# Kernel optimization log

Hardware: AMD Instinct MI355X
Metric: run time of the kernel (lower is better)

Reference implementation:

```python
import jax, jax.numpy as jnp
import numpy as np

BN_EPS = 1e-5

def _bn_train(h, gamma, beta):
    # BatchNorm1d in training mode: biased batch stats over the edge (batch) dim
    mean = jnp.mean(h, axis=0)
    var = jnp.var(h, axis=0)
    return (h - mean) * jax.lax.rsqrt(var + BN_EPS) * gamma + beta

def setup_inputs() -> dict:
    key = jax.random.key(0)
    ks = jax.random.split(key, 8)
    N, C, E = 50000, 128, 600000
    x = jax.random.normal(ks[0], (N, C), dtype=jnp.float32)
    edge_index = jax.random.randint(ks[1], (2, E), 0, N, dtype=jnp.int64)
    # Linear params, Kaiming-uniform-ish scale (values don't matter for correctness)
    def lin(k, fan_in, fan_out):
        k1, k2 = jax.random.split(k)
        bound = 1.0 / np.sqrt(fan_in)
        W = jax.random.uniform(k1, (fan_out, fan_in), jnp.float32, -bound, bound)
        b = jax.random.uniform(k2, (fan_out,), jnp.float32, -bound, bound)
        return W, b
    W1, b1 = lin(ks[2], 2 * C, C)
    W2, b2 = lin(ks[3], C, C)
    W3, b3 = lin(ks[4], C, 1)
    g1 = jnp.ones((C,), jnp.float32); be1 = jnp.zeros((C,), jnp.float32)
    g2 = jnp.ones((C,), jnp.float32); be2 = jnp.zeros((C,), jnp.float32)
    return {"x": x, "edge_index": edge_index,
            "W1": W1, "b1": b1, "g1": g1, "be1": be1,
            "W2": W2, "b2": b2, "g2": g2, "be2": be2,
            "W3": W3, "b3": b3}

def reference(x, edge_index, W1, b1, g1, be1, W2, b2, g2, be2, W3, b3):
    # gather endpoint features and concat: [E, 2C]
    ef = jnp.concatenate([x[edge_index[0]], x[edge_index[1]]], axis=1)
    h = jnp.einsum('ec,oc->eo', ef, W1) + b1          # [E, C]
    h = jax.nn.relu(_bn_train(h, g1, be1))
    h = jnp.einsum('ec,oc->eo', h, W2) + b2           # [E, C]
    h = jax.nn.relu(_bn_train(h, g2, be2))
    h = jnp.einsum('ec,oc->eo', h, W3) + b3           # [E, 1]
    return jnp.squeeze(h)                             # [E]
```

## Files before the change

kernel.cpp:

```cpp
#include <hip/hip_runtime.h>
#include <hip/hip_bf16.h>

#define CH 128

constexpr float BN_EPS = 1e-5f;

typedef short bf16x8 __attribute__((ext_vector_type(8)));
typedef float f32x4  __attribute__((ext_vector_type(4)));

__device__ __forceinline__ unsigned cvtpk_bf16(float lo, float hi) {
    unsigned r;
    asm("v_cvt_pk_bf16_f32 %0, %1, %2" : "=v"(r) : "v"(lo), "v"(hi));
    return r;
}
__device__ __forceinline__ float bf2f_lo(unsigned u) { return __uint_as_float(u << 16); }
__device__ __forceinline__ float bf2f_hi(unsigned u) { return __uint_as_float(u & 0xffff0000u); }

union BF8 { bf16x8 v; unsigned u[4]; };

__device__ __forceinline__ bf16x8 pack8(float f0, float f1, float f2, float f3,
                                        float f4, float f5, float f6, float f7) {
    BF8 r;
    r.u[0] = cvtpk_bf16(f0, f1);
    r.u[1] = cvtpk_bf16(f2, f3);
    r.u[2] = cvtpk_bf16(f4, f5);
    r.u[3] = cvtpk_bf16(f6, f7);
    return r.v;
}

__global__ __launch_bounds__(512, 4) void node_linear_kernel(
    const float* __restrict__ x, const float* __restrict__ W1,
    unsigned short* __restrict__ u_bf, unsigned short* __restrict__ v_bf, int N)
{
    __shared__ short xs[64 * 128];

    const int t = threadIdx.x;
    const int lane = t & 63;
    const int wv = t >> 6;
    const int l15 = lane & 15;
    const int l4 = lane >> 4;
    const int n0 = blockIdx.x * 64;

    bf16x8 wfrag[2][4];
    #pragma unroll
    for (int ot = 0; ot < 2; ++ot) {
        const int o_ = wv * 32 + ot * 16 + l15;
        const float* wrow = (o_ < 128) ? (W1 + (size_t)o_ * 256)
                                       : (W1 + (size_t)(o_ - 128) * 256 + 128);
        #pragma unroll
        for (int kk = 0; kk < 4; ++kk) {
            float4 a = *(const float4*)(wrow + kk * 32 + l4 * 8);
            float4 b = *(const float4*)(wrow + kk * 32 + l4 * 8 + 4);
            wfrag[ot][kk] = pack8(a.x, a.y, a.z, a.w, b.x, b.y, b.z, b.w);
        }
    }

    const int c16 = t & 15;
    const int cb = c16 * 8;
    const int nsl = t >> 4;
    #pragma unroll
    for (int nn = 0; nn < 2; ++nn) {
        const int n_loc = nsl + nn * 32;
        const int n = n0 + n_loc;
        bf16x8 xv = {0, 0, 0, 0, 0, 0, 0, 0};
        if (n < N) {
            float4 a = *(const float4*)(x + (size_t)n * CH + cb);
            float4 b = *(const float4*)(x + (size_t)n * CH + cb + 4);
            xv = pack8(a.x, a.y, a.z, a.w, b.x, b.y, b.z, b.w);
        }
        *(bf16x8*)(xs + n_loc * 128 + (c16 ^ (n_loc & 7)) * 8) = xv;
    }
    __syncthreads();

    unsigned short* ob = (wv < 4) ? u_bf : v_bf;
    const int chb = (wv & 3) * 32;

    #pragma unroll
    for (int g = 0; g < 4; ++g) {
        const int nrow = g * 16 + l15;
        f32x4 D0 = {0.f, 0.f, 0.f, 0.f};
        f32x4 D1 = {0.f, 0.f, 0.f, 0.f};
        #pragma unroll
        for (int kk = 0; kk < 4; ++kk) {
            bf16x8 a = *(const bf16x8*)(xs + nrow * 128 + ((kk * 4 + l4) ^ (l15 & 7)) * 8);
            D0 = __builtin_amdgcn_mfma_f32_16x16x32_bf16(a, wfrag[0][kk], D0, 0, 0, 0);
            D1 = __builtin_amdgcn_mfma_f32_16x16x32_bf16(a, wfrag[1][kk], D1, 0, 0, 0);
        }
        #pragma unroll
        for (int r = 0; r < 4; ++r) {
            const int n = n0 + g * 16 + l4 * 4 + r;
            if (n < N) {
                unsigned pk = cvtpk_bf16(D0[r], D1[r]);
                ob[(size_t)n * CH + chb + l15]      = (unsigned short)pk;
                ob[(size_t)n * CH + chb + 16 + l15] = (unsigned short)(pk >> 16);
            }
        }
    }
}

__global__ __launch_bounds__(256) void stats1_kernel(
    const unsigned short* __restrict__ u_bf, const unsigned short* __restrict__ v_bf,
    const int* __restrict__ src, const int* __restrict__ dst,
    float* __restrict__ partials, int E)
{
    const int t = threadIdx.x;
    const int c8 = t & 31;
    const int eslot = t >> 5;
    const uint2* u2 = (const uint2*)u_bf;
    const uint2* v2 = (const uint2*)v_bf;

    float rs0=0.f, rs1=0.f, rs2=0.f, rs3=0.f;
    float rq0=0.f, rq1=0.f, rq2=0.f, rq3=0.f;

    const int iters = (E + 7) >> 3;
    for (int it = blockIdx.x; it < iters; it += gridDim.x) {
        int e = it * 8 + eslot;
        if (e < E) {
            int s = src[e], d = dst[e];
            uint2 a = u2[(size_t)s * 32 + c8];
            uint2 b = v2[(size_t)d * 32 + c8];
            float h0 = bf2f_lo(a.x) + bf2f_lo(b.x);
            float h1 = bf2f_hi(a.x) + bf2f_hi(b.x);
            float h2 = bf2f_lo(a.y) + bf2f_lo(b.y);
            float h3 = bf2f_hi(a.y) + bf2f_hi(b.y);
            rs0 += h0; rq0 += h0 * h0;
            rs1 += h1; rq1 += h1 * h1;
            rs2 += h2; rq2 += h2 * h2;
            rs3 += h3; rq3 += h3 * h3;
        }
    }
    __shared__ float red[256];
    red[t] = 0.f;
    __syncthreads();
    int c = c8 * 4;
    atomicAdd(&red[c + 0], rs0); atomicAdd(&red[c + 1], rs1);
    atomicAdd(&red[c + 2], rs2); atomicAdd(&red[c + 3], rs3);
    atomicAdd(&red[128 + c + 0], rq0); atomicAdd(&red[128 + c + 1], rq1);
    atomicAdd(&red[128 + c + 2], rq2); atomicAdd(&red[128 + c + 3], rq3);
    __syncthreads();
    partials[(size_t)blockIdx.x * 256 + t] = red[t];
}

__global__ __launch_bounds__(1024) void finalize_kernel(
    const float* __restrict__ partials, int nblocks,
    const float* __restrict__ gamma, const float* __restrict__ beta,
    const float* __restrict__ bias,
    float* __restrict__ scale, float* __restrict__ shift, float invE)
{
    __shared__ float accs[1024], accq[1024];
    const int t = threadIdx.x;
    const int ch = t & 127;
    const int sl = t >> 7;
    float s = 0.f, q = 0.f;
    for (int b = sl; b < nblocks; b += 8) {
        s += partials[(size_t)b * 256 + ch];
        q += partials[(size_t)b * 256 + 128 + ch];
    }
    accs[t] = s; accq[t] = q;
    __syncthreads();
    if (t < 128) {
        float st = 0.f, qt = 0.f;
        #pragma unroll
        for (int k = 0; k < 8; ++k) { st += accs[k * 128 + t]; qt += accq[k * 128 + t]; }
        const float m0 = st * invE;
        const float var = fmaxf(qt * invE - m0 * m0, 0.f);
        const float mean = m0 + (bias ? bias[t] : 0.f);
        const float sc = gamma[t] * rsqrtf(var + BN_EPS);
        scale[t] = sc;
        shift[t] = beta[t] - mean * sc;
    }
}

__global__ __launch_bounds__(512, 4) void layer2_kernel(
    const unsigned short* __restrict__ u_bf, const unsigned short* __restrict__ v_bf,
    const int* __restrict__ src, const int* __restrict__ dst,
    const float* __restrict__ b1,
    const float* __restrict__ scale1, const float* __restrict__ shift1,
    const float* __restrict__ W2, const float* __restrict__ b2,
    uint2* __restrict__ h2raw, float* __restrict__ partials, int E)
{
    __shared__ short ybuf[64 * 128];
    __shared__ float red[256];

    const int t = threadIdx.x;
    const int lane = t & 63;
    const int wv = t >> 6;
    const int p = wv & 3;
    const int h = wv >> 2;
    const int l15 = lane & 15;
    const int l4  = lane >> 4;

    bf16x8 wfrag[2][4];
    #pragma unroll
    for (int ot = 0; ot < 2; ++ot) {
        const int o = p * 32 + ot * 16 + l15;
        #pragma unroll
        for (int kk = 0; kk < 4; ++kk) {
            const float* wp = W2 + (size_t)o * CH + kk * 32 + l4 * 8;
            float4 a = *(const float4*)wp;
            float4 bq = *(const float4*)(wp + 4);
            wfrag[ot][kk] = pack8(a.x, a.y, a.z, a.w, bq.x, bq.y, bq.z, bq.w);
        }
    }
    float b2r[2][4];
    #pragma unroll
    for (int ot = 0; ot < 2; ++ot)
        #pragma unroll
        for (int r = 0; r < 4; ++r)
            b2r[ot][r] = b2[p * 32 + ot * 16 + l4 * 4 + r];

    const int c16 = t & 15;
    const int cb = c16 * 8;
    const int ebase = t >> 4;
    const float4 sca = *(const float4*)(scale1 + cb);
    const float4 scb = *(const float4*)(scale1 + cb + 4);
    const float4 sha = *(const float4*)(shift1 + cb);
    const float4 shb = *(const float4*)(shift1 + cb + 4);
    const float4 b1a = *(const float4*)(b1 + cb);
    const float4 b1b = *(const float4*)(b1 + cb + 4);
    float4 bsa, bsb;
    bsa.x = b1a.x*sca.x + sha.x; bsa.y = b1a.y*sca.y + sha.y;
    bsa.z = b1a.z*sca.z + sha.z; bsa.w = b1a.w*sca.w + sha.w;
    bsb.x = b1b.x*scb.x + shb.x; bsb.y = b1b.y*scb.y + shb.y;
    bsb.z = b1b.z*scb.z + shb.z; bsb.w = b1b.w*scb.w + shb.w;

    float rs[2][4] = {{0.f,0.f,0.f,0.f},{0.f,0.f,0.f,0.f}};
    float rq[2][4] = {{0.f,0.f,0.f,0.f},{0.f,0.f,0.f,0.f}};

    const int ntiles = (E + 63) >> 6;
    for (int tile = blockIdx.x; tile < ntiles; tile += gridDim.x) {
        __syncthreads();
        #pragma unroll
        for (int ee = 0; ee < 2; ++ee) {
            const int e_loc = ebase + ee * 32;
            const int e = tile * 64 + e_loc;
            bf16x8 y8 = {0, 0, 0, 0, 0, 0, 0, 0};
            if (e < E) {
                const int s = src[e], d = dst[e];
                const uint4 ua = *(const uint4*)(u_bf + (size_t)s * CH + cb);
                const uint4 va = *(const uint4*)(v_bf + (size_t)d * CH + cb);
                const float f0 = bf2f_lo(ua.x) + bf2f_lo(va.x);
                const float f1 = bf2f_hi(ua.x) + bf2f_hi(va.x);
                const float f2 = bf2f_lo(ua.y) + bf2f_lo(va.y);
                const float f3 = bf2f_hi(ua.y) + bf2f_hi(va.y);
                const float f4 = bf2f_lo(ua.z) + bf2f_lo(va.z);
                const float f5 = bf2f_hi(ua.z) + bf2f_hi(va.z);
                const float f6 = bf2f_lo(ua.w) + bf2f_lo(va.w);
                const float f7 = bf2f_hi(ua.w) + bf2f_hi(va.w);
                y8 = pack8(fmaxf(f0 * sca.x + bsa.x, 0.f),
                           fmaxf(f1 * sca.y + bsa.y, 0.f),
                           fmaxf(f2 * sca.z + bsa.z, 0.f),
                           fmaxf(f3 * sca.w + bsa.w, 0.f),
                           fmaxf(f4 * scb.x + bsb.x, 0.f),
                           fmaxf(f5 * scb.y + bsb.y, 0.f),
                           fmaxf(f6 * scb.z + bsb.z, 0.f),
                           fmaxf(f7 * scb.w + bsb.w, 0.f));
            }
            *(bf16x8*)(ybuf + e_loc * 128 + (c16 ^ (e_loc & 7)) * 8) = y8;
        }
        __syncthreads();

        #pragma unroll
        for (int g2 = 0; g2 < 2; ++g2) {
            const int g = h * 2 + g2;
            const int erow = g * 16 + l15;
            f32x4 D0 = {0.f, 0.f, 0.f, 0.f};
            f32x4 D1 = {0.f, 0.f, 0.f, 0.f};
            #pragma unroll
            for (int kk = 0; kk < 4; ++kk) {
                bf16x8 yf = *(const bf16x8*)(ybuf + erow * 128 + ((kk * 4 + l4) ^ (l15 & 7)) * 8);
                D0 = __builtin_amdgcn_mfma_f32_16x16x32_bf16(wfrag[0][kk], yf, D0, 0, 0, 0);
                D1 = __builtin_amdgcn_mfma_f32_16x16x32_bf16(wfrag[1][kk], yf, D1, 0, 0, 0);
            }
            const int gblk = tile * 4 + g;
            const bool ev = ((size_t)gblk * 16 + l15) < (size_t)E;
            {
                const float a0 = D0[0] + b2r[0][0], a1 = D0[1] + b2r[0][1];
                const float a2 = D0[2] + b2r[0][2], a3 = D0[3] + b2r[0][3];
                rs[0][0] += ev ? a0 : 0.f; rq[0][0] += ev ? a0 * a0 : 0.f;
                rs[0][1] += ev ? a1 : 0.f; rq[0][1] += ev ? a1 * a1 : 0.f;
                rs[0][2] += ev ? a2 : 0.f; rq[0][2] += ev ? a2 * a2 : 0.f;
                rs[0][3] += ev ? a3 : 0.f; rq[0][3] += ev ? a3 * a3 : 0.f;
                h2raw[((size_t)gblk * 8 + p * 2 + 0) * 64 + lane] =
                    make_uint2(cvtpk_bf16(a0, a1), cvtpk_bf16(a2, a3));
            }
            {
                const float c0 = D1[0] + b2r[1][0], c1 = D1[1] + b2r[1][1];
                const float c2 = D1[2] + b2r[1][2], c3 = D1[3] + b2r[1][3];
                rs[1][0] += ev ? c0 : 0.f; rq[1][0] += ev ? c0 * c0 : 0.f;
                rs[1][1] += ev ? c1 : 0.f; rq[1][1] += ev ? c1 * c1 : 0.f;
                rs[1][2] += ev ? c2 : 0.f; rq[1][2] += ev ? c2 * c2 : 0.f;
                rs[1][3] += ev ? c3 : 0.f; rq[1][3] += ev ? c3 * c3 : 0.f;
                h2raw[((size_t)gblk * 8 + p * 2 + 1) * 64 + lane] =
                    make_uint2(cvtpk_bf16(c0, c1), cvtpk_bf16(c2, c3));
            }
        }
    }

    __syncthreads();
    if (t < 256) red[t] = 0.f;
    __syncthreads();
    #pragma unroll
    for (int ot = 0; ot < 2; ++ot) {
        #pragma unroll
        for (int r = 0; r < 4; ++r) {
            float a = rs[ot][r], b = rq[ot][r];
            #pragma unroll
            for (int m = 1; m <= 8; m <<= 1) {
                a += __shfl_xor(a, m, 64);
                b += __shfl_xor(b, m, 64);
            }
            if (l15 == 0) {
                const int ch = p * 32 + ot * 16 + l4 * 4 + r;
                atomicAdd(&red[ch], a);
                atomicAdd(&red[128 + ch], b);
            }
        }
    }
    __syncthreads();
    if (t < 256) partials[(size_t)blockIdx.x * 256 + t] = red[t];
}

__global__ __launch_bounds__(256) void output_kernel(
    const uint2* __restrict__ h2raw,
    const float* __restrict__ scale2, const float* __restrict__ shift2,
    const float* __restrict__ W3, const float* __restrict__ b3,
    float* __restrict__ out, int E)
{
    __shared__ float sc_s[128], sh_s[128], w3_s[128];
    const int t = threadIdx.x;
    if (t < 128) { sc_s[t] = scale2[t]; sh_s[t] = shift2[t]; w3_s[t] = W3[t]; }
    __syncthreads();
    const int wv = t >> 6;
    const int lane = t & 63;
    const int l15 = lane & 15;
    const int l4 = lane >> 4;
    const float bias = b3[0];
    const int ngrp = (E + 15) >> 4;
    for (int g = blockIdx.x * 4 + wv; g < ngrp; g += gridDim.x * 4) {
        float acc = 0.f;
        #pragma unroll
        for (int w = 0; w < 8; ++w) {
            uint2 raw = h2raw[((size_t)g * 8 + w) * 64 + lane];
            const int o = w * 16 + l4 * 4;
            float4 sc = *(const float4*)(sc_s + o);
            float4 sh = *(const float4*)(sh_s + o);
            float4 w3 = *(const float4*)(w3_s + o);
            float h0 = bf2f_lo(raw.x), h1 = bf2f_hi(raw.x);
            float h2 = bf2f_lo(raw.y), h3 = bf2f_hi(raw.y);
            acc += fmaxf(h0 * sc.x + sh.x, 0.f) * w3.x;
            acc += fmaxf(h1 * sc.y + sh.y, 0.f) * w3.y;
            acc += fmaxf(h2 * sc.z + sh.z, 0.f) * w3.z;
            acc += fmaxf(h3 * sc.w + sh.w, 0.f) * w3.w;
        }
        acc += __shfl_xor(acc, 16, 64);
        acc += __shfl_xor(acc, 32, 64);
        const int e = g * 16 + l15;
        if (l4 == 0 && e < E) out[e] = acc + bias;
    }
}

extern "C" void kernel_launch(void* const* d_in, const int* in_sizes, int n_in,
                              void* d_out, int out_size, void* d_ws, size_t ws_size,
                              hipStream_t stream)
{
    const float* x   = (const float*)d_in[0];
    const int*   ei  = (const int*)d_in[1];
    const float* W1  = (const float*)d_in[2];
    const float* b1  = (const float*)d_in[3];
    const float* g1  = (const float*)d_in[4];
    const float* be1 = (const float*)d_in[5];
    const float* W2  = (const float*)d_in[6];
    const float* b2  = (const float*)d_in[7];
    const float* g2  = (const float*)d_in[8];
    const float* be2 = (const float*)d_in[9];
    const float* W3  = (const float*)d_in[10];
    const float* b3  = (const float*)d_in[11];

    const int N = in_sizes[0] / CH;
    const int E = out_size;
    const int* src = ei;
    const int* dst = ei + E;

    const int S1_BLOCKS = 2048;
    const int S2_BLOCKS = 1024;
    const size_t ngblk = (size_t)((E + 63) >> 6) * 4;

    unsigned short* u_bf = (unsigned short*)d_ws;
    unsigned short* v_bf = u_bf + (size_t)N * CH;
    uint2* h2raw = (uint2*)(v_bf + (size_t)N * CH);
    float* part1 = (float*)(h2raw + ngblk * 8 * 64);
    float* part2 = part1 + (size_t)S1_BLOCKS * 256;
    float* scale1 = part2 + (size_t)S2_BLOCKS * 256;
    float* shift1 = scale1 + CH;
    float* scale2 = shift1 + CH;
    float* shift2 = scale2 + CH;
    float* out = (float*)d_out;

    node_linear_kernel<<<(N + 63) / 64, 512, 0, stream>>>(x, W1, u_bf, v_bf, N);
    stats1_kernel<<<S1_BLOCKS, 256, 0, stream>>>(u_bf, v_bf, src, dst, part1, E);
    finalize_kernel<<<1, 1024, 0, stream>>>(part1, S1_BLOCKS, g1, be1, b1,
                                            scale1, shift1, 1.0f / (float)E);
    layer2_kernel<<<S2_BLOCKS, 512, 0, stream>>>(u_bf, v_bf, src, dst, b1, scale1, shift1,
                                                 W2, b2, h2raw, part2, E);
    finalize_kernel<<<1, 1024, 0, stream>>>(part2, S2_BLOCKS, g2, be2, nullptr,
                                            scale2, shift2, 1.0f / (float)E);
    output_kernel<<<2048, 256, 0, stream>>>(h2raw, scale2, shift2, W3, b3, out, E);
}
```

Measured before the change: 314.1 us.

## Prefetch next-tile gathers with double-buffered LDS in layer2; unroll stats and output loops

```diff
diff --git a/kernel.cpp b/kernel.cpp
--- a/kernel.cpp
+++ b/kernel.cpp
@@ -15,6 +15,10 @@
 }
 __device__ __forceinline__ float bf2f_lo(unsigned u) { return __uint_as_float(u << 16); }
 __device__ __forceinline__ float bf2f_hi(unsigned u) { return __uint_as_float(u & 0xffff0000u); }
+
+__device__ __forceinline__ void lds_barrier() {
+    asm volatile("s_waitcnt lgkmcnt(0)\n\ts_barrier" ::: "memory");
+}
 
 union BF8 { bf16x8 v; unsigned u[4]; };
 
@@ -112,27 +116,35 @@
     float rs0=0.f, rs1=0.f, rs2=0.f, rs3=0.f;
     float rq0=0.f, rq1=0.f, rq2=0.f, rq3=0.f;
 
-    const int iters = (E + 7) >> 3;
+    const int iters = (E + 15) >> 4;
     for (int it = blockIdx.x; it < iters; it += gridDim.x) {
-        int e = it * 8 + eslot;
-        if (e < E) {
-            int s = src[e], d = dst[e];
-            uint2 a = u2[(size_t)s * 32 + c8];
-            uint2 b = v2[(size_t)d * 32 + c8];
-            float h0 = bf2f_lo(a.x) + bf2f_lo(b.x);
-            float h1 = bf2f_hi(a.x) + bf2f_hi(b.x);
-            float h2 = bf2f_lo(a.y) + bf2f_lo(b.y);
-            float h3 = bf2f_hi(a.y) + bf2f_hi(b.y);
-            rs0 += h0; rq0 += h0 * h0;
-            rs1 += h1; rq1 += h1 * h1;
-            rs2 += h2; rq2 += h2 * h2;
-            rs3 += h3; rq3 += h3 * h3;
+        const int e0 = it * 16 + eslot;
+        const int e1 = e0 + 8;
+        if (e0 < E) {
+            const int s = src[e0], d = dst[e0];
+            const uint2 a = u2[(size_t)s * 32 + c8];
+            const uint2 b = v2[(size_t)d * 32 + c8];
+            float h;
+            h = bf2f_lo(a.x) + bf2f_lo(b.x); rs0 += h; rq0 += h * h;
+            h = bf2f_hi(a.x) + bf2f_hi(b.x); rs1 += h; rq1 += h * h;
+            h = bf2f_lo(a.y) + bf2f_lo(b.y); rs2 += h; rq2 += h * h;
+            h = bf2f_hi(a.y) + bf2f_hi(b.y); rs3 += h; rq3 += h * h;
+        }
+        if (e1 < E) {
+            const int s = src[e1], d = dst[e1];
+            const uint2 a = u2[(size_t)s * 32 + c8];
+            const uint2 b = v2[(size_t)d * 32 + c8];
+            float h;
+            h = bf2f_lo(a.x) + bf2f_lo(b.x); rs0 += h; rq0 += h * h;
+            h = bf2f_hi(a.x) + bf2f_hi(b.x); rs1 += h; rq1 += h * h;
+            h = bf2f_lo(a.y) + bf2f_lo(b.y); rs2 += h; rq2 += h * h;
+            h = bf2f_hi(a.y) + bf2f_hi(b.y); rs3 += h; rq3 += h * h;
         }
     }
     __shared__ float red[256];
     red[t] = 0.f;
     __syncthreads();
-    int c = c8 * 4;
+    const int c = c8 * 4;
     atomicAdd(&red[c + 0], rs0); atomicAdd(&red[c + 1], rs1);
     atomicAdd(&red[c + 2], rs2); atomicAdd(&red[c + 3], rs3);
     atomicAdd(&red[128 + c + 0], rq0); atomicAdd(&red[128 + c + 1], rq1);
@@ -179,7 +191,7 @@
     const float* __restrict__ W2, const float* __restrict__ b2,
     uint2* __restrict__ h2raw, float* __restrict__ partials, int E)
 {
-    __shared__ short ybuf[64 * 128];
+    __shared__ short ybuf[2][64 * 128];
     __shared__ float red[256];
 
     const int t = threadIdx.x;
@@ -228,25 +240,37 @@
     float rq[2][4] = {{0.f,0.f,0.f,0.f},{0.f,0.f,0.f,0.f}};
 
     const int ntiles = (E + 63) >> 6;
-    for (int tile = blockIdx.x; tile < ntiles; tile += gridDim.x) {
-        __syncthreads();
-        #pragma unroll
-        for (int ee = 0; ee < 2; ++ee) {
-            const int e_loc = ebase + ee * 32;
-            const int e = tile * 64 + e_loc;
+    const int tstep = gridDim.x;
+
+    uint4 ua0, va0, ua1, va1;
+    int tile = blockIdx.x;
+    if (tile < ntiles) {
+        const int eA = tile * 64 + ebase;
+        const int eB = eA + 32;
+        const int cA = eA < E ? eA : E - 1;
+        const int cB = eB < E ? eB : E - 1;
+        const int sA = src[cA], dA = dst[cA];
+        const int sB = src[cB], dB = dst[cB];
+        ua0 = *(const uint4*)(u_bf + (size_t)sA * CH + cb);
+        va0 = *(const uint4*)(v_bf + (size_t)dA * CH + cb);
+        ua1 = *(const uint4*)(u_bf + (size_t)sB * CH + cb);
+        va1 = *(const uint4*)(v_bf + (size_t)dB * CH + cb);
+    }
+
+    int cur = 0;
+    for (; tile < ntiles; tile += tstep) {
+        {
+            const int e = tile * 64 + ebase;
             bf16x8 y8 = {0, 0, 0, 0, 0, 0, 0, 0};
             if (e < E) {
-                const int s = src[e], d = dst[e];
-                const uint4 ua = *(const uint4*)(u_bf + (size_t)s * CH + cb);
-                const uint4 va = *(const uint4*)(v_bf + (size_t)d * CH + cb);
-                const float f0 = bf2f_lo(ua.x) + bf2f_lo(va.x);
-                const float f1 = bf2f_hi(ua.x) + bf2f_hi(va.x);
-                const float f2 = bf2f_lo(ua.y) + bf2f_lo(va.y);
-                const float f3 = bf2f_hi(ua.y) + bf2f_hi(va.y);
-                const float f4 = bf2f_lo(ua.z) + bf2f_lo(va.z);
-                const float f5 = bf2f_hi(ua.z) + bf2f_hi(va.z);
-                const float f6 = bf2f_lo(ua.w) + bf2f_lo(va.w);
-                const float f7 = bf2f_hi(ua.w) + bf2f_hi(va.w);
+                const float f0 = bf2f_lo(ua0.x) + bf2f_lo(va0.x);
+                const float f1 = bf2f_hi(ua0.x) + bf2f_hi(va0.x);
+                const float f2 = bf2f_lo(ua0.y) + bf2f_lo(va0.y);
+                const float f3 = bf2f_hi(ua0.y) + bf2f_hi(va0.y);
+                const float f4 = bf2f_lo(ua0.z) + bf2f_lo(va0.z);
+                const float f5 = bf2f_hi(ua0.z) + bf2f_hi(va0.z);
+                const float f6 = bf2f_lo(ua0.w) + bf2f_lo(va0.w);
+                const float f7 = bf2f_hi(ua0.w) + bf2f_hi(va0.w);
                 y8 = pack8(fmaxf(f0 * sca.x + bsa.x, 0.f),
                            fmaxf(f1 * sca.y + bsa.y, 0.f),
                            fmaxf(f2 * sca.z + bsa.z, 0.f),
@@ -256,9 +280,48 @@
                            fmaxf(f6 * scb.z + bsb.z, 0.f),
                            fmaxf(f7 * scb.w + bsb.w, 0.f));
             }
-            *(bf16x8*)(ybuf + e_loc * 128 + (c16 ^ (e_loc & 7)) * 8) = y8;
-        }
-        __syncthreads();
+            *(bf16x8*)(ybuf[cur] + ebase * 128 + (c16 ^ (ebase & 7)) * 8) = y8;
+        }
+        {
+            const int e_loc = ebase + 32;
+            const int e = tile * 64 + e_loc;
+            bf16x8 y8 = {0, 0, 0, 0, 0, 0, 0, 0};
+            if (e < E) {
+                const float f0 = bf2f_lo(ua1.x) + bf2f_lo(va1.x);
+                const float f1 = bf2f_hi(ua1.x) + bf2f_hi(va1.x);
+                const float f2 = bf2f_lo(ua1.y) + bf2f_lo(va1.y);
+                const float f3 = bf2f_hi(ua1.y) + bf2f_hi(va1.y);
+                const float f4 = bf2f_lo(ua1.z) + bf2f_lo(va1.z);
+                const float f5 = bf2f_hi(ua1.z) + bf2f_hi(va1.z);
+                const float f6 = bf2f_lo(ua1.w) + bf2f_lo(va1.w);
+                const float f7 = bf2f_hi(ua1.w) + bf2f_hi(va1.w);
+                y8 = pack8(fmaxf(f0 * sca.x + bsa.x, 0.f),
+                           fmaxf(f1 * sca.y + bsa.y, 0.f),
+                           fmaxf(f2 * sca.z + bsa.z, 0.f),
+                           fmaxf(f3 * sca.w + bsa.w, 0.f),
+                           fmaxf(f4 * scb.x + bsb.x, 0.f),
+                           fmaxf(f5 * scb.y + bsb.y, 0.f),
+                           fmaxf(f6 * scb.z + bsb.z, 0.f),
+                           fmaxf(f7 * scb.w + bsb.w, 0.f));
+            }
+            *(bf16x8*)(ybuf[cur] + e_loc * 128 + (c16 ^ (ebase & 7)) * 8) = y8;
+        }
+
+        const int ntile = tile + tstep;
+        if (ntile < ntiles) {
+            const int eA = ntile * 64 + ebase;
+            const int eB = eA + 32;
+            const int cA = eA < E ? eA : E - 1;
+            const int cB = eB < E ? eB : E - 1;
+            const int sA = src[cA], dA = dst[cA];
+            const int sB = src[cB], dB = dst[cB];
+            ua0 = *(const uint4*)(u_bf + (size_t)sA * CH + cb);
+            va0 = *(const uint4*)(v_bf + (size_t)dA * CH + cb);
+            ua1 = *(const uint4*)(u_bf + (size_t)sB * CH + cb);
+            va1 = *(const uint4*)(v_bf + (size_t)dB * CH + cb);
+        }
+
+        lds_barrier();
 
         #pragma unroll
         for (int g2 = 0; g2 < 2; ++g2) {
@@ -268,7 +331,7 @@
             f32x4 D1 = {0.f, 0.f, 0.f, 0.f};
             #pragma unroll
             for (int kk = 0; kk < 4; ++kk) {
-                bf16x8 yf = *(const bf16x8*)(ybuf + erow * 128 + ((kk * 4 + l4) ^ (l15 & 7)) * 8);
+                bf16x8 yf = *(const bf16x8*)(ybuf[cur] + erow * 128 + ((kk * 4 + l4) ^ (l15 & 7)) * 8);
                 D0 = __builtin_amdgcn_mfma_f32_16x16x32_bf16(wfrag[0][kk], yf, D0, 0, 0, 0);
                 D1 = __builtin_amdgcn_mfma_f32_16x16x32_bf16(wfrag[1][kk], yf, D1, 0, 0, 0);
             }
@@ -295,6 +358,7 @@
                     make_uint2(cvtpk_bf16(c0, c1), cvtpk_bf16(c2, c3));
             }
         }
+        cur ^= 1;
     }
 
     __syncthreads();
@@ -337,26 +401,48 @@
     const int l4 = lane >> 4;
     const float bias = b3[0];
     const int ngrp = (E + 15) >> 4;
-    for (int g = blockIdx.x * 4 + wv; g < ngrp; g += gridDim.x * 4) {
-        float acc = 0.f;
+    const int gstep = gridDim.x * 4;
+    for (int g0 = blockIdx.x * 4 + wv; g0 < ngrp; g0 += 2 * gstep) {
+        const int g1 = g0 + gstep;
+        float acc0 = 0.f, acc1 = 0.f;
         #pragma unroll
         for (int w = 0; w < 8; ++w) {
-            uint2 raw = h2raw[((size_t)g * 8 + w) * 64 + lane];
+            const uint2 raw = h2raw[((size_t)g0 * 8 + w) * 64 + lane];
             const int o = w * 16 + l4 * 4;
-            float4 sc = *(const float4*)(sc_s + o);
-            float4 sh = *(const float4*)(sh_s + o);
-            float4 w3 = *(const float4*)(w3_s + o);
-            float h0 = bf2f_lo(raw.x), h1 = bf2f_hi(raw.x);
-            float h2 = bf2f_lo(raw.y), h3 = bf2f_hi(raw.y);
-            acc += fmaxf(h0 * sc.x + sh.x, 0.f) * w3.x;
-            acc += fmaxf(h1 * sc.y + sh.y, 0.f) * w3.y;
-            acc += fmaxf(h2 * sc.z + sh.z, 0.f) * w3.z;
-            acc += fmaxf(h3 * sc.w + sh.w, 0.f) * w3.w;
-        }
-        acc += __shfl_xor(acc, 16, 64);
-        acc += __shfl_xor(acc, 32, 64);
-        const int e = g * 16 + l15;
-        if (l4 == 0 && e < E) out[e] = acc + bias;
+            const float4 sc = *(const float4*)(sc_s + o);
+            const float4 sh = *(const float4*)(sh_s + o);
+            const float4 w3 = *(const float4*)(w3_s + o);
+            acc0 += fmaxf(bf2f_lo(raw.x) * sc.x + sh.x, 0.f) * w3.x;
+            acc0 += fmaxf(bf2f_hi(raw.x) * sc.y + sh.y, 0.f) * w3.y;
+            acc0 += fmaxf(bf2f_lo(raw.y) * sc.z + sh.z, 0.f) * w3.z;
+            acc0 += fmaxf(bf2f_hi(raw.y) * sc.w + sh.w, 0.f) * w3.w;
+        }
+        if (g1 < ngrp) {
+            #pragma unroll
+            for (int w = 0; w < 8; ++w) {
+                const uint2 raw = h2raw[((size_t)g1 * 8 + w) * 64 + lane];
+                const int o = w * 16 + l4 * 4;
+                const float4 sc = *(const float4*)(sc_s + o);
+                const float4 sh = *(const float4*)(sh_s + o);
+                const float4 w3 = *(const float4*)(w3_s + o);
+                acc1 += fmaxf(bf2f_lo(raw.x) * sc.x + sh.x, 0.f) * w3.x;
+                acc1 += fmaxf(bf2f_hi(raw.x) * sc.y + sh.y, 0.f) * w3.y;
+                acc1 += fmaxf(bf2f_lo(raw.y) * sc.z + sh.z, 0.f) * w3.z;
+                acc1 += fmaxf(bf2f_hi(raw.y) * sc.w + sh.w, 0.f) * w3.w;
+            }
+        }
+        acc0 += __shfl_xor(acc0, 16, 64);
+        acc0 += __shfl_xor(acc0, 32, 64);
+        acc1 += __shfl_xor(acc1, 16, 64);
+        acc1 += __shfl_xor(acc1, 32, 64);
+        if (l4 == 0) {
+            const int e0 = g0 * 16 + l15;
+            if (e0 < E) out[e0] = acc0 + bias;
+            if (g1 < ngrp) {
+                const int e1 = g1 * 16 + l15;
+                if (e1 < E) out[e1] = acc1 + bias;
+            }
+        }
     }
 }
 
```

Result: no change. 307.9 us (-2.0%).
